# Optimization experiments

Hardware: AMD Instinct MI355X
Metric: run time of the kernel (lower is better)

The kernel has to match this reference:

```python
import jax, jax.numpy as jnp
import numpy as np

E = 8          # num_experts
K = 2          # top_k
CAPF = 1.25    # capacity_factor
DIM = 512
HID = 2048     # int(dim * mlp_ratio)


def setup_inputs() -> dict:
    key = jax.random.key(0)
    ks = jax.random.split(key, 5)
    s = 0.02
    x = jax.random.normal(ks[0], (8, 2048, DIM), jnp.float32)
    Wr = jax.random.normal(ks[1], (E, DIM), jnp.float32) * s          # router weight (no bias)
    W1 = jax.random.normal(ks[2], (E, HID, DIM), jnp.float32) * s     # fc1 weights per expert
    b1 = jnp.zeros((E, HID), jnp.float32)
    W2 = jax.random.normal(ks[3], (E, DIM, HID), jnp.float32) * s     # fc2 weights per expert
    b2 = jnp.zeros((E, DIM), jnp.float32)
    return {"x": x, "Wr": Wr, "W1": W1, "b1": b1, "W2": W2, "b2": b2}


def _capacity_keep(top_w, top_idx, cap):
    """For each (slot, expert), keep only the `cap` highest-weight tokens.
    top_w, top_idx: [T, K]. Returns bool keep mask [T, K]."""
    def per_slot(w, idx):
        order = jnp.argsort(-w)                       # tokens sorted by weight desc
        idx_sorted = idx[order]                       # [T] expert id in sorted order
        oh = jax.nn.one_hot(idx_sorted, E, dtype=jnp.int32)
        rank = jnp.cumsum(oh, axis=0) - 1             # rank within each expert
        r = jnp.take_along_axis(rank, idx_sorted[:, None], axis=1)[:, 0]
        keep_sorted = r < cap
        return jnp.zeros(w.shape[0], bool).at[order].set(keep_sorted)
    return jax.vmap(per_slot, in_axes=(1, 1), out_axes=1)(top_w, top_idx)


def reference(x, Wr, W1, b1, W2, b2):
    b, n, d = x.shape
    T = b * n
    flat = x.reshape(T, d)

    # Router: softmax in fp32 then cast back
    logits = flat @ Wr.T                                            # [T, E]
    probs = jax.nn.softmax(logits.astype(jnp.float32), axis=-1).astype(flat.dtype)
    top_w, top_idx = jax.lax.top_k(probs, K)                        # [T, K]
    top_w = top_w / (jnp.sum(top_w, axis=-1, keepdims=True) + 1e-8)

    # Capacity-limited drop, then renormalize
    cap = max(1, int(CAPF * T * K / E))
    keep = _capacity_keep(top_w, top_idx, cap)
    top_w = jnp.where(keep, top_w, 0.0)
    top_w = top_w / jnp.clip(jnp.sum(top_w, axis=-1, keepdims=True), 1e-8, None)

    # Combine weight per (token, expert): scatter-add top_w into dense [T, E]
    rows = jnp.arange(T)[:, None]
    w_te = jnp.zeros((T, E), flat.dtype).at[rows, top_idx].add(top_w)

    # Per-expert MLP, weighted combine (w_te is 0 for unassigned/dropped pairs)
    out = jnp.zeros_like(flat)
    for e in range(E):
        h = jax.nn.gelu(flat @ W1[e].T + b1[e], approximate=False)  # [T, HID]
        y = h @ W2[e].T + b2[e]                                     # [T, D]
        out = out + w_te[:, e:e + 1] * y

    # Load-balancing aux loss
    load = jnp.sum(w_te, axis=0) / T
    importance = probs.mean(0)
    aux = jnp.sum(importance * load * float(E))
    return out.reshape(b, n, d), aux
```

## Files before the change

### kernel.cpp

```cpp
#include <hip/hip_runtime.h>
#include <hip/hip_bf16.h>
#include <math.h>

#define DIM 512
#define HID 2048
#define NE  8
#define CSTRIDE 32

typedef __attribute__((ext_vector_type(8))) short short8;
typedef __attribute__((ext_vector_type(4))) float f32x4;
typedef unsigned short ushort_t;

static __device__ __forceinline__ ushort_t f2bf(float f) {
    unsigned int x = __builtin_bit_cast(unsigned int, f);
    unsigned int lsb = (x >> 16) & 1u;
    x += 0x7fffu + lsb;
    return (ushort_t)(x >> 16);
}
static __device__ __forceinline__ float bf2f(ushort_t u) {
    unsigned int x = ((unsigned int)u) << 16;
    return __builtin_bit_cast(float, x);
}

static __device__ __forceinline__ float fast_gelu(float v) {
    float u = v * 0.70710678118654752f;
    float s = fabsf(u);
    float t = __builtin_amdgcn_rcpf(1.f + 0.3275911f * s);
    float poly = ((((1.061405429f * t - 1.453152027f) * t + 1.421413741f) * t
                   - 0.284496736f) * t + 0.254829592f) * t;
    float e = __expf(-s * s);
    float erfv = copysignf(1.f - poly * e, u);
    return 0.5f * v * (1.f + erfv);
}

static __device__ __forceinline__ void gld16(const void* g, void* l) {
    __builtin_amdgcn_global_load_lds(
        (const __attribute__((address_space(1))) void*)g,
        (__attribute__((address_space(3))) void*)l,
        16, 0, 0);
}

__global__ void k_cvt2(const float* __restrict__ s1, ushort_t* __restrict__ d1, int n1,
                       const float* __restrict__ s2, ushort_t* __restrict__ d2, int n2) {
    int i = blockIdx.x * blockDim.x + threadIdx.x;
    int stride = gridDim.x * blockDim.x;
    int n4a = n1 >> 2, n4b = n2 >> 2;
    for (int j = i; j < n4a; j += stride) {
        float4 v = ((const float4*)s1)[j];
        ushort4 o;
        o.x = f2bf(v.x); o.y = f2bf(v.y); o.z = f2bf(v.z); o.w = f2bf(v.w);
        ((ushort4*)d1)[j] = o;
    }
    for (int j = i; j < n4b; j += stride) {
        float4 v = ((const float4*)s2)[j];
        ushort4 o;
        o.x = f2bf(v.x); o.y = f2bf(v.y); o.z = f2bf(v.z); o.w = f2bf(v.w);
        ((ushort4*)d2)[j] = o;
    }
}

__global__ __launch_bounds__(256) void k_router(const float* __restrict__ x,
    const float* __restrict__ Wr, ushort_t* __restrict__ xb,
    float* __restrict__ probs, int* __restrict__ tidx, float* __restrict__ tw, int T)
{
    int lane = threadIdx.x & 63;
    int t = blockIdx.x * 4 + (threadIdx.x >> 6);
    if (t >= T) return;
    const float* xr = x + (size_t)t * DIM;
    double acc[NE];
#pragma unroll
    for (int e = 0; e < NE; e++) acc[e] = 0.0;
    for (int i = lane; i < DIM; i += 64) {
        float xv = xr[i];
        xb[(size_t)t * DIM + i] = f2bf(xv);
        double xd = (double)xv;
#pragma unroll
        for (int e = 0; e < NE; e++) acc[e] += xd * (double)Wr[e * DIM + i];
    }
#pragma unroll
    for (int e = 0; e < NE; e++) {
#pragma unroll
        for (int off = 32; off > 0; off >>= 1) acc[e] += __shfl_xor(acc[e], off);
    }
    double mx = acc[0];
#pragma unroll
    for (int e = 1; e < NE; e++) mx = fmax(mx, acc[e]);
    double p[NE], sum = 0.0;
#pragma unroll
    for (int e = 0; e < NE; e++) { p[e] = exp(acc[e] - mx); sum += p[e]; }
    float pr[NE];
#pragma unroll
    for (int e = 0; e < NE; e++) pr[e] = (float)(p[e] / sum);
    if (lane < NE) probs[(size_t)t * NE + lane] = pr[lane];
    if (lane == 0) {
        int i1 = 0; float b1v = pr[0];
#pragma unroll
        for (int e = 1; e < NE; e++) if (pr[e] > b1v) { b1v = pr[e]; i1 = e; }
        int i2 = -1; float b2v = -1.f;
#pragma unroll
        for (int e = 0; e < NE; e++) if (e != i1 && pr[e] > b2v) { b2v = pr[e]; i2 = e; }
        float s2 = b1v + b2v + 1e-8f;
        tidx[t * 2] = i1; tidx[t * 2 + 1] = i2;
        tw[t * 2] = b1v / s2; tw[t * 2 + 1] = b2v / s2;
    }
}

__global__ __launch_bounds__(256) void k_hist(const int* __restrict__ tidx,
                                              int* __restrict__ cnt, int T) {
    __shared__ int h[16];
    if (threadIdx.x < 16) h[threadIdx.x] = 0;
    __syncthreads();
    int stride = gridDim.x * blockDim.x;
    for (int t = blockIdx.x * blockDim.x + threadIdx.x; t < T; t += stride) {
        atomicAdd(&h[tidx[t * 2]], 1);
        atomicAdd(&h[8 + tidx[t * 2 + 1]], 1);
    }
    __syncthreads();
    if (threadIdx.x < 16 && h[threadIdx.x] != 0)
        atomicAdd(&cnt[threadIdx.x * CSTRIDE], h[threadIdx.x]);
}

__global__ __launch_bounds__(256) void k_post(const int* __restrict__ tidx,
        const float* __restrict__ tw, const int* __restrict__ cnt,
        const float* __restrict__ probs, int* __restrict__ lcnt,
        int* __restrict__ ltok, int* __restrict__ pos, float* __restrict__ tw2,
        float* __restrict__ partial, int T, int cap, int capM)
{
    __shared__ int h[NE];
    __shared__ int base[NE];
    __shared__ float red[256 * 16];
    if (threadIdx.x < NE) h[threadIdx.x] = 0;
    __syncthreads();
    int t = blockIdx.x * blockDim.x + threadIdx.x;
    float wkn[2] = {0.f, 0.f};
    int myE[2] = {-1, -1};
    int myp[2] = {0, 0};
    if (t < T) {
        float wk[2]; int es[2];
#pragma unroll
        for (int s = 0; s < 2; s++) {
            int e = tidx[t * 2 + s];
            float w = tw[t * 2 + s];
            es[s] = e; wk[s] = w;
            if (cnt[(s * NE + e) * CSTRIDE] > cap) {
                int rank = 0;
                for (int t2 = 0; t2 < T; t2++) {
                    if (tidx[t2 * 2 + s] == e) {
                        float w2 = tw[t2 * 2 + s];
                        if (w2 > w || (w2 == w && t2 < t)) rank++;
                    }
                }
                if (rank >= cap) wk[s] = 0.f;
            }
        }
        float denom = fmaxf(wk[0] + wk[1], 1e-8f);
#pragma unroll
        for (int s = 0; s < 2; s++) {
            wkn[s] = wk[s] / denom;
            tw2[t * 2 + s] = wkn[s];
            if (wkn[s] != 0.f) {
                myE[s] = es[s];
                myp[s] = atomicAdd(&h[es[s]], 1);
            }
        }
    }
    __syncthreads();
    if (threadIdx.x < NE)
        base[threadIdx.x] = (h[threadIdx.x] != 0)
            ? atomicAdd(&lcnt[threadIdx.x * CSTRIDE], h[threadIdx.x]) : 0;
    __syncthreads();
    float imp[NE], ld[NE];
#pragma unroll
    for (int e = 0; e < NE; e++) { imp[e] = 0.f; ld[e] = 0.f; }
    if (t < T) {
#pragma unroll
        for (int s = 0; s < 2; s++) {
            if (myE[s] >= 0) {
                int p = base[myE[s]] + myp[s];
                ltok[myE[s] * capM + p] = t;
                pos[t * 2 + s] = (myE[s] << 20) | p;
                ld[myE[s]] += wkn[s];
            } else {
                pos[t * 2 + s] = -1;
            }
        }
#pragma unroll
        for (int e = 0; e < NE; e++) imp[e] = probs[(size_t)t * NE + e];
    }
#pragma unroll
    for (int e = 0; e < NE; e++) {
        red[threadIdx.x * 16 + e] = imp[e];
        red[threadIdx.x * 16 + 8 + e] = ld[e];
    }
    __syncthreads();
    for (int off = 128; off > 0; off >>= 1) {
        if (threadIdx.x < off) {
#pragma unroll
            for (int j = 0; j < 16; j++)
                red[threadIdx.x * 16 + j] += red[(threadIdx.x + off) * 16 + j];
        }
        __syncthreads();
    }
    if (threadIdx.x < 16) partial[blockIdx.x * 16 + threadIdx.x] = red[threadIdx.x];
}

__global__ void k_tail(const int* __restrict__ lcnt, int* __restrict__ loff,
                       const float* __restrict__ partial, float* __restrict__ outaux,
                       int nb, int T)
{
    __shared__ float s[16];
    if (threadIdx.x == 0) {
        int o = 0;
        for (int e = 0; e < NE; e++) {
            loff[e] = o;
            o += ((lcnt[e * CSTRIDE] + 255) >> 8) << 8;
        }
        loff[NE] = o;
    }
    if (threadIdx.x < 16) {
        float a = 0.f;
        for (int b = 0; b < nb; b++) a += partial[b * 16 + threadIdx.x];
        s[threadIdx.x] = a;
    }
    __syncthreads();
    if (threadIdx.x == 0) {
        float invT = 1.f / (float)T;
        float aux = 0.f;
        for (int e = 0; e < NE; e++)
            aux += (s[e] * invT) * (s[8 + e] * invT) * (float)NE;
        outaux[0] = aux;
    }
}

__global__ __launch_bounds__(512, 4) void k_fc1(
    const ushort_t* __restrict__ xb, const ushort_t* __restrict__ W1b,
    const float* __restrict__ b1, const int* __restrict__ lcnt,
    const int* __restrict__ loff, const int* __restrict__ ltok,
    ushort_t* __restrict__ hbuf, int capM)
{
    int bx = blockIdx.x;
    int e  = bx & 7;
    int r  = bx >> 3;
    int mt = r >> 4;
    int nt = r & 15;
    int cnt = lcnt[e * CSTRIDE];
    if (cnt > capM) cnt = capM;
    int m0 = mt * 256;
    if (m0 >= cnt) return;
    int n0 = nt * 128;
    const int* toks = ltok + e * capM;
    int hrow0 = loff[e] + m0;
    const ushort_t* Bsrc = W1b + (size_t)e * HID * DIM;

    __shared__ char smem[49152];
    char* As = smem;
    char* Bs = smem + 32768;

    int tid = threadIdx.x;
    int wave = tid >> 6, lane = tid & 63;
    int wm = wave >> 1, wn = wave & 1;

    const char* aSrc[4]; int aldst[4];
#pragma unroll
    for (int i = 0; i < 4; i++) {
        int c = tid + 512 * i;
        int row = c >> 3, cc = c & 7;
        int scc = cc ^ (row & 7);
        int gr = m0 + row;
        int tok = toks[gr < cnt ? gr : (cnt - 1)];
        aSrc[i] = (const char*)(xb + (size_t)tok * DIM + scc * 8);
        aldst[i] = (wave * 64 + 512 * i) * 16;
    }
    const char* bSrc[2]; int bldst[2];
#pragma unroll
    for (int i = 0; i < 2; i++) {
        int c = tid + 512 * i;
        int row = c >> 3, cc = c & 7;
        int scc = cc ^ (row & 7);
        bSrc[i] = (const char*)(Bsrc + (size_t)(n0 + row) * DIM + scc * 8);
        bldst[i] = (wave * 64 + 512 * i) * 16;
    }

    f32x4 acc[4][4];
#pragma unroll
    for (int a = 0; a < 4; a++)
#pragma unroll
        for (int b = 0; b < 4; b++) acc[a][b] = (f32x4){0.f, 0.f, 0.f, 0.f};

    int aRow = wm * 64 + (lane & 15);
    int bRow = wn * 64 + (lane & 15);
    int kq = lane >> 4;
    int swz0 = (kq ^ (lane & 7)) << 4;
    int swz1 = ((4 + kq) ^ (lane & 7)) << 4;
    int aoff[2] = { aRow * 128 + swz0, aRow * 128 + swz1 };
    int boff[2] = { bRow * 128 + swz0, bRow * 128 + swz1 };

    auto STAGE = [&](int kofs) {
#pragma unroll
        for (int i = 0; i < 4; i++) gld16(aSrc[i] + kofs, As + aldst[i]);
#pragma unroll
        for (int i = 0; i < 2; i++) gld16(bSrc[i] + kofs, Bs + bldst[i]);
    };
    auto COMPUTE = [&]() {
#pragma unroll
        for (int kk = 0; kk < 2; kk++) {
            short8 af[4], bfr[4];
#pragma unroll
            for (int mf = 0; mf < 4; mf++)
                af[mf] = *(const short8*)(As + aoff[kk] + mf * 2048);
#pragma unroll
            for (int nf = 0; nf < 4; nf++)
                bfr[nf] = *(const short8*)(Bs + boff[kk] + nf * 2048);
#pragma unroll
            for (int mf = 0; mf < 4; mf++)
#pragma unroll
                for (int nf = 0; nf < 4; nf++)
                    acc[mf][nf] = __builtin_amdgcn_mfma_f32_16x16x32_bf16(bfr[nf], af[mf], acc[mf][nf], 0, 0, 0);
        }
    };

#pragma unroll
    for (int kt = 0; kt < DIM / 64; kt++) {
        STAGE(kt * 128);
        __syncthreads();
        COMPUTE();
        __syncthreads();
    }

    const float* b1e = b1 + e * HID;
    int mlocal = wm * 64 + (lane & 15);
    int nbase0 = n0 + wn * 64 + (lane >> 4) * 4;
#pragma unroll
    for (int mf = 0; mf < 4; mf++) {
        int mrow = mlocal + mf * 16;
        bool valid = (m0 + mrow) < cnt;
        ushort_t* dst = hbuf + (size_t)(hrow0 + mrow) * HID;
#pragma unroll
        for (int nf = 0; nf < 4; nf++) {
            int nc = nbase0 + nf * 16;
            float4 bias4 = *(const float4*)(b1e + nc);
            ushort4 o;
            o.x = f2bf(fast_gelu(acc[mf][nf][0] + bias4.x));
            o.y = f2bf(fast_gelu(acc[mf][nf][1] + bias4.y));
            o.z = f2bf(fast_gelu(acc[mf][nf][2] + bias4.z));
            o.w = f2bf(fast_gelu(acc[mf][nf][3] + bias4.w));
            if (valid) *(ushort4*)(dst + nc) = o;
        }
    }
}

__global__ __launch_bounds__(512, 4) void k_fc2(
    const ushort_t* __restrict__ hbuf, const ushort_t* __restrict__ W2b,
    const float* __restrict__ b2, const int* __restrict__ lcnt,
    const int* __restrict__ loff, ushort_t* __restrict__ ybuf, int capM)
{
    int bx = blockIdx.x;
    int e  = bx & 7;
    int r  = bx >> 3;
    int mt = r >> 2;
    int nt = r & 3;
    int cnt = lcnt[e * CSTRIDE];
    if (cnt > capM) cnt = capM;
    int m0 = mt * 256;
    if (m0 >= cnt) return;
    int n0 = nt * 128;
    int hrow0 = loff[e] + m0;
    const ushort_t* Bsrc = W2b + (size_t)e * DIM * HID;

    __shared__ char smem[49152];
    char* As = smem;
    char* Bs = smem + 32768;

    int tid = threadIdx.x;
    int wave = tid >> 6, lane = tid & 63;
    int wm = wave >> 1, wn = wave & 1;

    const char* aSrc[4]; int aldst[4];
#pragma unroll
    for (int i = 0; i < 4; i++) {
        int c = tid + 512 * i;
        int row = c >> 3, cc = c & 7;
        int scc = cc ^ (row & 7);
        aSrc[i] = (const char*)(hbuf + (size_t)(hrow0 + row) * HID + scc * 8);
        aldst[i] = (wave * 64 + 512 * i) * 16;
    }
    const char* bSrc[2]; int bldst[2];
#pragma unroll
    for (int i = 0; i < 2; i++) {
        int c = tid + 512 * i;
        int row = c >> 3, cc = c & 7;
        int scc = cc ^ (row & 7);
        bSrc[i] = (const char*)(Bsrc + (size_t)(n0 + row) * HID + scc * 8);
        bldst[i] = (wave * 64 + 512 * i) * 16;
    }

    f32x4 acc[4][4];
#pragma unroll
    for (int a = 0; a < 4; a++)
#pragma unroll
        for (int b = 0; b < 4; b++) acc[a][b] = (f32x4){0.f, 0.f, 0.f, 0.f};

    int aRow = wm * 64 + (lane & 15);
    int bRow = wn * 64 + (lane & 15);
    int kq = lane >> 4;
    int swz0 = (kq ^ (lane & 7)) << 4;
    int swz1 = ((4 + kq) ^ (lane & 7)) << 4;
    int aoff[2] = { aRow * 128 + swz0, aRow * 128 + swz1 };
    int boff[2] = { bRow * 128 + swz0, bRow * 128 + swz1 };

    auto STAGE = [&](int kofs) {
#pragma unroll
        for (int i = 0; i < 4; i++) gld16(aSrc[i] + kofs, As + aldst[i]);
#pragma unroll
        for (int i = 0; i < 2; i++) gld16(bSrc[i] + kofs, Bs + bldst[i]);
    };
    auto COMPUTE = [&]() {
#pragma unroll
        for (int kk = 0; kk < 2; kk++) {
            short8 af[4], bfr[4];
#pragma unroll
            for (int mf = 0; mf < 4; mf++)
                af[mf] = *(const short8*)(As + aoff[kk] + mf * 2048);
#pragma unroll
            for (int nf = 0; nf < 4; nf++)
                bfr[nf] = *(const short8*)(Bs + boff[kk] + nf * 2048);
#pragma unroll
            for (int mf = 0; mf < 4; mf++)
#pragma unroll
                for (int nf = 0; nf < 4; nf++)
                    acc[mf][nf] = __builtin_amdgcn_mfma_f32_16x16x32_bf16(bfr[nf], af[mf], acc[mf][nf], 0, 0, 0);
        }
    };

    for (int kg = 0; kg < 4; kg++) {
#pragma unroll
        for (int k8 = 0; k8 < 8; k8++) {
            STAGE(k8 * 128);
            __syncthreads();
            COMPUTE();
            __syncthreads();
        }
#pragma unroll
        for (int i = 0; i < 4; i++) aSrc[i] += 1024;
#pragma unroll
        for (int i = 0; i < 2; i++) bSrc[i] += 1024;
    }

    const float* b2e = b2 + e * DIM;
    int mlocal = wm * 64 + (lane & 15);
    int nbase0 = n0 + wn * 64 + (lane >> 4) * 4;
#pragma unroll
    for (int mf = 0; mf < 4; mf++) {
        int mrow = mlocal + mf * 16;
        bool valid = (m0 + mrow) < cnt;
        ushort_t* dst = ybuf + (size_t)(hrow0 + mrow) * DIM;
#pragma unroll
        for (int nf = 0; nf < 4; nf++) {
            int nc = nbase0 + nf * 16;
            float4 bias4 = *(const float4*)(b2e + nc);
            ushort4 o;
            o.x = f2bf(acc[mf][nf][0] + bias4.x);
            o.y = f2bf(acc[mf][nf][1] + bias4.y);
            o.z = f2bf(acc[mf][nf][2] + bias4.z);
            o.w = f2bf(acc[mf][nf][3] + bias4.w);
            if (valid) *(ushort4*)(dst + nc) = o;
        }
    }
}

__global__ __launch_bounds__(256) void k_comb(const ushort_t* __restrict__ ybuf,
    const float* __restrict__ tw2, const int* __restrict__ pos,
    const int* __restrict__ loff, float* __restrict__ out, int T, int capM)
{
    int wv = threadIdx.x >> 6, lane = threadIdx.x & 63;
    int t = blockIdx.x * 4 + wv;
    if (t >= T) return;
    float o[8];
#pragma unroll
    for (int j = 0; j < 8; j++) o[j] = 0.f;
#pragma unroll
    for (int s = 0; s < 2; s++) {
        int pk = pos[t * 2 + s];
        if (pk >= 0) {
            float w = tw2[t * 2 + s];
            int e = pk >> 20, p = pk & 0xFFFFF;
            int row = loff[e] + p;
            short8 y = *(const short8*)(ybuf + (size_t)row * DIM + lane * 8);
#pragma unroll
            for (int j = 0; j < 8; j++) o[j] += w * bf2f((ushort_t)y[j]);
        }
    }
    float4* dst = (float4*)(out + (size_t)t * DIM + lane * 8);
    dst[0] = (float4){o[0], o[1], o[2], o[3]};
    dst[1] = (float4){o[4], o[5], o[6], o[7]};
}

extern "C" void kernel_launch(void* const* d_in, const int* in_sizes, int n_in,
                              void* d_out, int out_size, void* d_ws, size_t ws_size,
                              hipStream_t stream)
{
    const float* x  = (const float*)d_in[0];
    const float* Wr = (const float*)d_in[1];
    const float* W1 = (const float*)d_in[2];
    const float* b1 = (const float*)d_in[3];
    const float* W2 = (const float*)d_in[4];
    const float* b2 = (const float*)d_in[5];
    float* out = (float*)d_out;

    int T = in_sizes[0] / DIM;
    int cap = (int)(1.25 * (double)T * 2.0 / 8.0);
    if (cap < 1) cap = 1;
    int capM = 2 * cap; if (capM > T) capM = T;
    int mtmax = (capM + 255) / 256;
    int nposts = (T + 255) / 256;

    char* w = (char*)d_ws;
    size_t off = 0;
    auto alloc = [&](size_t bytes) {
        char* p = w + off;
        off = (off + bytes + 255) & ~(size_t)255;
        return p;
    };
    size_t ybrows = (size_t)T * 2 + NE * 256;
    size_t ybbytes = ybrows * DIM * 2;
    ushort_t* ybuf = (ushort_t*)w;
    ushort_t* xb   = (ushort_t*)alloc((size_t)T * DIM * 2);
    ushort_t* W1b  = (ushort_t*)alloc((size_t)NE * HID * DIM * 2);
    if (off < ybbytes) off = (ybbytes + 255) & ~(size_t)255;
    ushort_t* W2b  = (ushort_t*)alloc((size_t)NE * DIM * HID * 2);
    ushort_t* hbuf = (ushort_t*)alloc(ybrows * HID * 2);
    float* probs   = (float*)alloc((size_t)T * NE * 4);
    int*   tidx    = (int*)alloc((size_t)T * 2 * 4);
    float* tw      = (float*)alloc((size_t)T * 2 * 4);
    float* tw2     = (float*)alloc((size_t)T * 2 * 4);
    int*   pos     = (int*)alloc((size_t)T * 2 * 4);
    int*   cnt     = (int*)alloc(16 * CSTRIDE * 4);
    int*   lcnt    = (int*)alloc(NE * CSTRIDE * 4);
    int*   loff    = (int*)alloc((NE + 1) * 4);
    int*   ltok    = (int*)alloc((size_t)NE * capM * 4);
    float* partial = (float*)alloc((size_t)nposts * 16 * 4);

    (void)hipMemsetAsync(cnt, 0, 16 * CSTRIDE * 4, stream);
    (void)hipMemsetAsync(lcnt, 0, NE * CSTRIDE * 4, stream);

    k_cvt2<<<2048, 256, 0, stream>>>(W1, W1b, NE * HID * DIM, W2, W2b, NE * DIM * HID);
    k_router<<<(T + 3) / 4, 256, 0, stream>>>(x, Wr, xb, probs, tidx, tw, T);
    k_hist<<<64, 256, 0, stream>>>(tidx, cnt, T);
    k_post<<<nposts, 256, 0, stream>>>(tidx, tw, cnt, probs, lcnt, ltok, pos, tw2,
                                       partial, T, cap, capM);
    k_tail<<<1, 64, 0, stream>>>(lcnt, loff, partial, out + (size_t)T * DIM, nposts, T);

    k_fc1<<<NE * mtmax * (HID / 128), 512, 0, stream>>>(
        xb, W1b, b1, lcnt, loff, ltok, hbuf, capM);
    k_fc2<<<NE * mtmax * (DIM / 128), 512, 0, stream>>>(
        hbuf, W2b, b2, lcnt, loff, ybuf, capM);
    k_comb<<<(T + 3) / 4, 256, 0, stream>>>(ybuf, tw2, pos, loff, out, T, capM);
}
```

Before: 317.9 us.

## Double-buffer LDS in expert GEMMs and shrink tiles to 128x128 with 256 threads

Both expert GEMM kernels (fc1 and fc2) now use two LDS buffers. The global-to-LDS loads for the next K tile are issued before computing the current one, with explicit vmcnt waits and raw barriers replacing the two __syncthreads per step. The M tile shrinks from 256 to 128 rows with 256-thread blocks, and expert padding in the row offsets is reduced to 128. The aim is to overlap memory latency with MFMA work and waste less compute on padded rows. The cost is 64KB of LDS per block, which limits occupancy, and reliance on hand-tuned waitcnt values.

```diff
diff --git a/kernel.cpp b/kernel.cpp
--- a/kernel.cpp
+++ b/kernel.cpp
@@ -213,7 +213,7 @@
         int o = 0;
         for (int e = 0; e < NE; e++) {
             loff[e] = o;
-            o += ((lcnt[e * CSTRIDE] + 255) >> 8) << 8;
+            o += ((lcnt[e * CSTRIDE] + 127) >> 7) << 7;
         }
         loff[NE] = o;
     }
@@ -232,7 +232,7 @@
     }
 }
 
-__global__ __launch_bounds__(512, 4) void k_fc1(
+__global__ __launch_bounds__(256, 2) void k_fc1(
     const ushort_t* __restrict__ xb, const ushort_t* __restrict__ W1b,
     const float* __restrict__ b1, const int* __restrict__ lcnt,
     const int* __restrict__ loff, const int* __restrict__ ltok,
@@ -245,40 +245,32 @@
     int nt = r & 15;
     int cnt = lcnt[e * CSTRIDE];
     if (cnt > capM) cnt = capM;
-    int m0 = mt * 256;
+    int m0 = mt * 128;
     if (m0 >= cnt) return;
     int n0 = nt * 128;
     const int* toks = ltok + e * capM;
     int hrow0 = loff[e] + m0;
     const ushort_t* Bsrc = W1b + (size_t)e * HID * DIM;
 
-    __shared__ char smem[49152];
-    char* As = smem;
-    char* Bs = smem + 32768;
+    __shared__ char smem[65536];
+    char* As0 = smem;          char* Bs0 = smem + 16384;
+    char* As1 = smem + 32768;  char* Bs1 = smem + 49152;
 
     int tid = threadIdx.x;
     int wave = tid >> 6, lane = tid & 63;
     int wm = wave >> 1, wn = wave & 1;
 
-    const char* aSrc[4]; int aldst[4];
+    const char* aSrc[4]; const char* bSrc[4]; int ldst[4];
 #pragma unroll
     for (int i = 0; i < 4; i++) {
-        int c = tid + 512 * i;
+        int c = tid + 256 * i;
         int row = c >> 3, cc = c & 7;
         int scc = cc ^ (row & 7);
         int gr = m0 + row;
         int tok = toks[gr < cnt ? gr : (cnt - 1)];
         aSrc[i] = (const char*)(xb + (size_t)tok * DIM + scc * 8);
-        aldst[i] = (wave * 64 + 512 * i) * 16;
-    }
-    const char* bSrc[2]; int bldst[2];
-#pragma unroll
-    for (int i = 0; i < 2; i++) {
-        int c = tid + 512 * i;
-        int row = c >> 3, cc = c & 7;
-        int scc = cc ^ (row & 7);
         bSrc[i] = (const char*)(Bsrc + (size_t)(n0 + row) * DIM + scc * 8);
-        bldst[i] = (wave * 64 + 512 * i) * 16;
+        ldst[i] = (i * 256 + wave * 64) * 16;
     }
 
     f32x4 acc[4][4];
@@ -295,22 +287,23 @@
     int aoff[2] = { aRow * 128 + swz0, aRow * 128 + swz1 };
     int boff[2] = { bRow * 128 + swz0, bRow * 128 + swz1 };
 
-    auto STAGE = [&](int kofs) {
-#pragma unroll
-        for (int i = 0; i < 4; i++) gld16(aSrc[i] + kofs, As + aldst[i]);
-#pragma unroll
-        for (int i = 0; i < 2; i++) gld16(bSrc[i] + kofs, Bs + bldst[i]);
+    auto STAGE = [&](int kofs, char* A, char* B) {
+#pragma unroll
+        for (int i = 0; i < 4; i++) {
+            gld16(aSrc[i] + kofs, A + ldst[i]);
+            gld16(bSrc[i] + kofs, B + ldst[i]);
+        }
     };
-    auto COMPUTE = [&]() {
+    auto COMPUTE = [&](const char* A, const char* B) {
 #pragma unroll
         for (int kk = 0; kk < 2; kk++) {
             short8 af[4], bfr[4];
 #pragma unroll
             for (int mf = 0; mf < 4; mf++)
-                af[mf] = *(const short8*)(As + aoff[kk] + mf * 2048);
+                af[mf] = *(const short8*)(A + aoff[kk] + mf * 2048);
 #pragma unroll
             for (int nf = 0; nf < 4; nf++)
-                bfr[nf] = *(const short8*)(Bs + boff[kk] + nf * 2048);
+                bfr[nf] = *(const short8*)(B + boff[kk] + nf * 2048);
 #pragma unroll
             for (int mf = 0; mf < 4; mf++)
 #pragma unroll
@@ -319,12 +312,23 @@
         }
     };
 
-#pragma unroll
-    for (int kt = 0; kt < DIM / 64; kt++) {
-        STAGE(kt * 128);
-        __syncthreads();
-        COMPUTE();
-        __syncthreads();
+    const int NT = DIM / 64;
+    STAGE(0, As0, Bs0);
+#pragma unroll
+    for (int t = 0; t < NT; t++) {
+        char* Ac = (t & 1) ? As1 : As0;
+        char* Bc = (t & 1) ? Bs1 : Bs0;
+        if (t + 1 < NT) {
+            STAGE((t + 1) * 128, (t & 1) ? As0 : As1, (t & 1) ? Bs0 : Bs1);
+            asm volatile("s_waitcnt vmcnt(8)" ::: "memory");
+        } else {
+            asm volatile("s_waitcnt vmcnt(0)" ::: "memory");
+        }
+        __builtin_amdgcn_s_barrier();
+        __builtin_amdgcn_sched_barrier(0);
+        COMPUTE(Ac, Bc);
+        __builtin_amdgcn_sched_barrier(0);
+        __builtin_amdgcn_s_barrier();
     }
 
     const float* b1e = b1 + e * HID;
@@ -349,7 +353,7 @@
     }
 }
 
-__global__ __launch_bounds__(512, 4) void k_fc2(
+__global__ __launch_bounds__(256, 2) void k_fc2(
     const ushort_t* __restrict__ hbuf, const ushort_t* __restrict__ W2b,
     const float* __restrict__ b2, const int* __restrict__ lcnt,
     const int* __restrict__ loff, ushort_t* __restrict__ ybuf, int capM)
@@ -361,37 +365,29 @@
     int nt = r & 3;
     int cnt = lcnt[e * CSTRIDE];
     if (cnt > capM) cnt = capM;
-    int m0 = mt * 256;
+    int m0 = mt * 128;
     if (m0 >= cnt) return;
     int n0 = nt * 128;
     int hrow0 = loff[e] + m0;
     const ushort_t* Bsrc = W2b + (size_t)e * DIM * HID;
 
-    __shared__ char smem[49152];
-    char* As = smem;
-    char* Bs = smem + 32768;
+    __shared__ char smem[65536];
+    char* As0 = smem;          char* Bs0 = smem + 16384;
+    char* As1 = smem + 32768;  char* Bs1 = smem + 49152;
 
     int tid = threadIdx.x;
     int wave = tid >> 6, lane = tid & 63;
     int wm = wave >> 1, wn = wave & 1;
 
-    const char* aSrc[4]; int aldst[4];
+    const char* aSrc[4]; const char* bSrc[4]; int ldst[4];
 #pragma unroll
     for (int i = 0; i < 4; i++) {
-        int c = tid + 512 * i;
+        int c = tid + 256 * i;
         int row = c >> 3, cc = c & 7;
         int scc = cc ^ (row & 7);
         aSrc[i] = (const char*)(hbuf + (size_t)(hrow0 + row) * HID + scc * 8);
-        aldst[i] = (wave * 64 + 512 * i) * 16;
-    }
-    const char* bSrc[2]; int bldst[2];
-#pragma unroll
-    for (int i = 0; i < 2; i++) {
-        int c = tid + 512 * i;
-        int row = c >> 3, cc = c & 7;
-        int scc = cc ^ (row & 7);
         bSrc[i] = (const char*)(Bsrc + (size_t)(n0 + row) * HID + scc * 8);
-        bldst[i] = (wave * 64 + 512 * i) * 16;
+        ldst[i] = (i * 256 + wave * 64) * 16;
     }
 
     f32x4 acc[4][4];
@@ -408,22 +404,23 @@
     int aoff[2] = { aRow * 128 + swz0, aRow * 128 + swz1 };
     int boff[2] = { bRow * 128 + swz0, bRow * 128 + swz1 };
 
-    auto STAGE = [&](int kofs) {
-#pragma unroll
-        for (int i = 0; i < 4; i++) gld16(aSrc[i] + kofs, As + aldst[i]);
-#pragma unroll
-        for (int i = 0; i < 2; i++) gld16(bSrc[i] + kofs, Bs + bldst[i]);
+    auto STAGE = [&](int kofs, char* A, char* B) {
+#pragma unroll
+        for (int i = 0; i < 4; i++) {
+            gld16(aSrc[i] + kofs, A + ldst[i]);
+            gld16(bSrc[i] + kofs, B + ldst[i]);
+        }
     };
-    auto COMPUTE = [&]() {
+    auto COMPUTE = [&](const char* A, const char* B) {
 #pragma unroll
         for (int kk = 0; kk < 2; kk++) {
             short8 af[4], bfr[4];
 #pragma unroll
             for (int mf = 0; mf < 4; mf++)
-                af[mf] = *(const short8*)(As + aoff[kk] + mf * 2048);
+                af[mf] = *(const short8*)(A + aoff[kk] + mf * 2048);
 #pragma unroll
             for (int nf = 0; nf < 4; nf++)
-                bfr[nf] = *(const short8*)(Bs + boff[kk] + nf * 2048);
+                bfr[nf] = *(const short8*)(B + boff[kk] + nf * 2048);
 #pragma unroll
             for (int mf = 0; mf < 4; mf++)
 #pragma unroll
@@ -432,18 +429,23 @@
         }
     };
 
-    for (int kg = 0; kg < 4; kg++) {
-#pragma unroll
-        for (int k8 = 0; k8 < 8; k8++) {
-            STAGE(k8 * 128);
-            __syncthreads();
-            COMPUTE();
-            __syncthreads();
-        }
-#pragma unroll
-        for (int i = 0; i < 4; i++) aSrc[i] += 1024;
-#pragma unroll
-        for (int i = 0; i < 2; i++) bSrc[i] += 1024;
+    const int NT = HID / 64;
+    STAGE(0, As0, Bs0);
+#pragma unroll
+    for (int t = 0; t < NT; t++) {
+        char* Ac = (t & 1) ? As1 : As0;
+        char* Bc = (t & 1) ? Bs1 : Bs0;
+        if (t + 1 < NT) {
+            STAGE((t + 1) * 128, (t & 1) ? As0 : As1, (t & 1) ? Bs0 : Bs1);
+            asm volatile("s_waitcnt vmcnt(8)" ::: "memory");
+        } else {
+            asm volatile("s_waitcnt vmcnt(0)" ::: "memory");
+        }
+        __builtin_amdgcn_s_barrier();
+        __builtin_amdgcn_sched_barrier(0);
+        COMPUTE(Ac, Bc);
+        __builtin_amdgcn_sched_barrier(0);
+        __builtin_amdgcn_s_barrier();
     }
 
     const float* b2e = b2 + e * DIM;
@@ -511,7 +513,7 @@
     int cap = (int)(1.25 * (double)T * 2.0 / 8.0);
     if (cap < 1) cap = 1;
     int capM = 2 * cap; if (capM > T) capM = T;
-    int mtmax = (capM + 255) / 256;
+    int mtmax = (capM + 127) / 128;
     int nposts = (T + 255) / 256;
 
     char* w = (char*)d_ws;
@@ -521,7 +523,7 @@
         off = (off + bytes + 255) & ~(size_t)255;
         return p;
     };
-    size_t ybrows = (size_t)T * 2 + NE * 256;
+    size_t ybrows = (size_t)T * 2 + NE * 128;
     size_t ybbytes = ybrows * DIM * 2;
     ushort_t* ybuf = (ushort_t*)w;
     ushort_t* xb   = (ushort_t*)alloc((size_t)T * DIM * 2);
@@ -550,9 +552,9 @@
                                        partial, T, cap, capM);
     k_tail<<<1, 64, 0, stream>>>(lcnt, loff, partial, out + (size_t)T * DIM, nposts, T);
 
-    k_fc1<<<NE * mtmax * (HID / 128), 512, 0, stream>>>(
+    k_fc1<<<NE * mtmax * (HID / 128), 256, 0, stream>>>(
         xb, W1b, b1, lcnt, loff, ltok, hbuf, capM);
-    k_fc2<<<NE * mtmax * (DIM / 128), 512, 0, stream>>>(
+    k_fc2<<<NE * mtmax * (DIM / 128), 256, 0, stream>>>(
         hbuf, W2b, b2, lcnt, loff, ybuf, capM);
     k_comb<<<(T + 3) / 4, 256, 0, stream>>>(ybuf, tw2, pos, loff, out, T, capM);
 }
```

Result: faster. 275.9 us (-13.2%).
